# Kernel optimization log

Hardware: AMD Instinct MI355X
Metric: run time of the kernel (lower is better)

## Reference

```python
import jax, jax.numpy as jnp
import numpy as np

H = 16      # num_attention_heads
D = 1024    # hidden_size
HD = D // H # head dim = 64
ALPHA = 0.5


def setup_inputs() -> dict:
    key = jax.random.key(0)
    ks = jax.random.split(key, 12)
    B, S = 4, 1024
    s = 0.02
    return {
        "hidden_states": jax.random.normal(ks[0], (B, S, D), jnp.float32),
        "attention_mask": jnp.zeros((B, 1, 1, S), jnp.float32),
        "previous_attention": jax.random.uniform(ks[1], (B, H, S, S), jnp.float32),
        "Wq": jax.random.normal(ks[2], (D, D), jnp.float32) * s,
        "bq": jnp.zeros((D,), jnp.float32),
        "Wk": jax.random.normal(ks[3], (D, D), jnp.float32) * s,
        "bk": jnp.zeros((D,), jnp.float32),
        "Wv": jax.random.normal(ks[4], (D, D), jnp.float32) * s,
        "bv": jnp.zeros((D,), jnp.float32),
        "Wc": jax.random.normal(ks[5], (H, H), jnp.float32) * 0.25,  # 1x1 conv head-mix weight
        "bc": jnp.zeros((H,), jnp.float32),
    }


def reference(hidden_states, attention_mask, previous_attention,
              Wq, bq, Wk, bk, Wv, bv, Wc, bc):
    B, S, _ = hidden_states.shape

    def heads(x):  # [B,S,D] -> [B,H,S,HD]
        return x.reshape(B, S, H, HD).transpose(0, 2, 1, 3)

    q = heads(hidden_states @ Wq.T + bq)
    k = heads(hidden_states @ Wk.T + bk)
    v = heads(hidden_states @ Wv.T + bv)

    scores = jnp.einsum("bhsd,bhtd->bhst", q, k) / np.sqrt(HD).astype(np.float32)
    scores = scores + attention_mask
    probs = jax.nn.softmax(scores, axis=-1)

    # 1x1 conv across head channels == head-mixing matmul, then blend + re-softmax
    mixed_prev = jnp.einsum("gh,bhst->bgst", Wc, previous_attention) + bc[None, :, None, None]
    probs = jax.nn.softmax(ALPHA * mixed_prev + (1.0 - ALPHA) * probs, axis=-1)
    # dropout p=0.0 -> identity (inference)

    ctx = jnp.einsum("bhst,bhtd->bhsd", probs, v)
    ctx = ctx.transpose(0, 2, 1, 3).reshape(B, S, D)
    return ctx
```

## Files before the change

kernel.cpp:

```cpp
#include <hip/hip_runtime.h>
#include <hip/hip_bf16.h>

typedef unsigned short u16;
typedef __attribute__((ext_vector_type(8))) short  bf16x8;
typedef __attribute__((ext_vector_type(4))) float  f32x4;
typedef __attribute__((ext_vector_type(4))) int    i32x4;
typedef __attribute__((ext_vector_type(4))) float  f32x4v;

#define MFMA16(a,b,c) __builtin_amdgcn_mfma_f32_16x16x32_bf16((a),(b),(c),0,0,0)


static constexpr size_t OFF_HBF = 0;
static constexpr size_t OFF_WBF = 8388608;
static constexpr size_t OFF_QKV = 14680064;
static constexpr size_t OFF_VT  = 39845888;
static constexpr size_t OFF_MIX = 48234496;

__device__ __forceinline__ u16 f2b(float f) {
  unsigned int u = __builtin_bit_cast(unsigned int, f);
  unsigned int r = (u + 0x7fffu + ((u >> 16) & 1u)) >> 16;
  return (u16)r;
}
__device__ __forceinline__ float b2f(u16 x) {
  union { unsigned int u; float f; } c; c.u = ((unsigned int)x) << 16; return c.f;
}

__device__ __forceinline__ void gload_lds16(const u16* g, u16* l) {
  __builtin_amdgcn_global_load_lds(
      (const __attribute__((address_space(1))) unsigned int*)g,
      (__attribute__((address_space(3))) unsigned int*)l, 16, 0, 0);
}

__global__ void __launch_bounds__(256) k_convert(
    const float* __restrict__ hid, const float* __restrict__ wq,
    const float* __restrict__ wk,  const float* __restrict__ wv,
    u16* __restrict__ hbf, u16* __restrict__ wbf)
{
  int i4 = blockIdx.x * 256 + threadIdx.x;
  f32x4v v; u16* dst;
  if (i4 < 1048576) {
    v = *(const f32x4v*)(hid + (size_t)i4 * 4);
    dst = hbf + (size_t)i4 * 4;
  } else {
    int j = (i4 - 1048576) * 4;
    const float* s = (j < 1048576) ? (wq + j)
                   : (j < 2097152) ? (wk + (j - 1048576))
                                   : (wv + (j - 2097152));
    v = *(const f32x4v*)s;
    dst = wbf + j;
  }
  u16 o[4];
  for (int k = 0; k < 4; ++k) o[k] = f2b(v[k]);
  *(unsigned long long*)dst = *(unsigned long long*)o;
}

__global__ void __launch_bounds__(256) k_qkv(
    const u16* __restrict__ Abf, const u16* __restrict__ Wbf,
    const float* __restrict__ bq, const float* __restrict__ bk,
    const float* __restrict__ bv, u16* __restrict__ qkv)
{
  __shared__ __align__(16) u16 As[2][128][32];
  __shared__ __align__(16) u16 Bs[2][128][32];
  const int n0 = blockIdx.x * 128;
  const int m0 = blockIdx.y * 128;
  const int tid = threadIdx.x;
  const int l = tid & 63, w = tid >> 6;
  const int lr = l & 15, lg = l >> 4;
  const int wm = (w >> 1) * 64, wn = (w & 1) * 64;
  const int sx = (lg ^ ((lr >> 1) & 3)) * 8;

  f32x4 acc[4][4] = {};

  auto issue = [&](int buf, int k0) {
#pragma unroll
    for (int i = 0; i < 2; ++i) {
      int c = tid + i * 256;
      int row = c >> 2, cc = c & 3;
      int gc = cc ^ ((row >> 1) & 3);
      gload_lds16(Abf + (size_t)(m0 + row) * 1024 + k0 + gc * 8, &As[buf][row][cc * 8]);
      gload_lds16(Wbf + (size_t)(n0 + row) * 1024 + k0 + gc * 8, &Bs[buf][row][cc * 8]);
    }
  };

  issue(0, 0);
  for (int k0 = 0; k0 < 1024; k0 += 32) {
    int kb = (k0 >> 5) & 1;
    __syncthreads();
    if (k0 + 32 < 1024) issue(kb ^ 1, k0 + 32);
    bf16x8 a[4], bb[4];
#pragma unroll
    for (int mi = 0; mi < 4; ++mi)
      a[mi] = *(const bf16x8*)(&As[kb][wm + mi * 16 + lr][sx]);
#pragma unroll
    for (int ni = 0; ni < 4; ++ni)
      bb[ni] = *(const bf16x8*)(&Bs[kb][wn + ni * 16 + lr][sx]);
#pragma unroll
    for (int mi = 0; mi < 4; ++mi)
#pragma unroll
      for (int ni = 0; ni < 4; ++ni)
        acc[mi][ni] = MFMA16(a[mi], bb[ni], acc[mi][ni]);
  }
#pragma unroll
  for (int mi = 0; mi < 4; ++mi)
#pragma unroll
    for (int ni = 0; ni < 4; ++ni) {
      int col = n0 + wn + ni * 16 + lr;
      const float* bias = (col < 1024) ? bq : (col < 2048) ? bk : bv;
      float bvv = bias[col & 1023];
      int rowb = m0 + wm + mi * 16 + lg * 4;
#pragma unroll
      for (int r = 0; r < 4; ++r)
        qkv[(size_t)(rowb + r) * 3072 + col] = f2b(acc[mi][ni][r] + bvv);
    }
}

__global__ void __launch_bounds__(256) k_vt(const u16* __restrict__ qkv,
                                            u16* __restrict__ vt)
{
  __shared__ __align__(16) u16 tile[64][68];
  int blk = blockIdx.x;
  int st = blk & 15, h = (blk >> 4) & 15, b = blk >> 8;
  int tid = threadIdx.x;
  for (int i = 0; i < 16; ++i) {
    int idx = tid + i * 256;
    int r = idx >> 6, c = idx & 63;
    tile[r][c] = qkv[(size_t)(b * 1024 + st * 64 + r) * 3072 + 2048 + h * 64 + c];
  }
  __syncthreads();
  for (int i = 0; i < 16; ++i) {
    int idx = tid + i * 256;
    int d = idx >> 6, s = idx & 63;
    vt[((size_t)(b * 16 + h) * 64 + d) * 1024 + st * 64 + s] = tile[s][d];
  }
}

__global__ void __launch_bounds__(256) k_mix(
    const float* __restrict__ prev, const float* __restrict__ Wc,
    const float* __restrict__ bc, u16* __restrict__ mixed)
{
  __shared__ float wcs[256];
  __shared__ float bcs[16];
  int bsi = blockIdx.x;
  int b = bsi >> 10, s = bsi & 1023;
  int tid = threadIdx.x;
  wcs[tid] = 0.5f * Wc[tid];
  if (tid < 16) bcs[tid] = 0.5f * bc[tid];
  __syncthreads();
  size_t base = (size_t)b * 16777216 + (size_t)s * 1024;
  int t = tid * 4;
  f32x4v p[16];
#pragma unroll
  for (int hh = 0; hh < 16; ++hh)
    p[hh] = *(const f32x4v*)(prev + base + (size_t)hh * 1048576 + t);
#pragma unroll
  for (int g = 0; g < 16; ++g) {
    float bg = bcs[g];
    f32x4v a = {bg, bg, bg, bg};
#pragma unroll
    for (int hh = 0; hh < 16; ++hh)
      a += p[hh] * wcs[g * 16 + hh];
    u16 o[4];
#pragma unroll
    for (int j = 0; j < 4; ++j) o[j] = f2b(a[j]);
    *(unsigned long long*)(mixed + base + (size_t)g * 1048576 + t) =
        *(unsigned long long*)o;
  }
}

__global__ void __launch_bounds__(256) k_attn(
    const u16* __restrict__ qkv, const u16* __restrict__ vt,
    const u16* __restrict__ mixed, const float* __restrict__ mask,
    float* __restrict__ out)
{
  __shared__ __align__(16) char smraw[32768];
  u16   (*sc)[1024]   = (u16 (*)[1024])smraw;
  float (*ctxw)[16][64] = (float (*)[16][64])smraw;
  __shared__ float lw[4][16], l1inv[16];

  int blk = blockIdx.x;
  int sb = blk & 63, bh = blk >> 6;
  int h = bh & 15, b = bh >> 4;
  int s0 = sb * 16;
  int tid = threadIdx.x;
  int l = tid & 63, w = tid >> 6;
  int lr = l & 15, lg = l >> 4;

  const size_t qrow = (size_t)(b * 1024 + s0 + lr) * 3072 + h * 64;
  bf16x8 aq0 = *(const bf16x8*)(qkv + qrow + lg * 8);
  bf16x8 aq1 = *(const bf16x8*)(qkv + qrow + 32 + lg * 8);

#pragma unroll
  for (int tf = 0; tf < 16; ++tf) {
    int trow = w * 256 + tf * 16 + lr;
    const size_t krow = (size_t)(b * 1024 + trow) * 3072 + 1024 + h * 64;
    bf16x8 bk0 = *(const bf16x8*)(qkv + krow + lg * 8);
    bf16x8 bk1 = *(const bf16x8*)(qkv + krow + 32 + lg * 8);
    f32x4 acc = {0.f, 0.f, 0.f, 0.f};
    acc = MFMA16(aq0, bk0, acc);
    acc = MFMA16(aq1, bk1, acc);
    float mk = mask[b * 1024 + trow];
#pragma unroll
    for (int r = 0; r < 4; ++r) {
      int row = lg * 4 + r;
      float sv = acc[r] * 0.125f + mk;
      int addr = (((trow >> 3) ^ (row & 7)) << 3) + (trow & 7);
      sc[row][addr] = f2b(sv);
    }
  }
  __syncthreads();

  {
    int row = tid >> 4, ch = tid & 15;
    float sm = 0.f;
#pragma unroll
    for (int c8 = 0; c8 < 8; ++c8) {
      int chunk = ch * 8 + c8;
      bf16x8 v = *(const bf16x8*)(&sc[row][(chunk ^ (row & 7)) << 3]);
#pragma unroll
      for (int j = 0; j < 8; ++j) sm += __expf(b2f((u16)v[j]));
    }
    for (int d = 8; d >= 1; d >>= 1) sm += __shfl_xor(sm, d);
    if (ch == 0) l1inv[row] = 1.0f / sm;
  }
  __syncthreads();

  float l1h = 0.5f * l1inv[lr];
  float l2 = 0.f;
  f32x4 cacc[4] = {};
  const size_t mixrow = ((size_t)(b * 16 + h) * 1024 + s0 + lr) * 1024;
  const size_t vbase = (size_t)(b * 16 + h) * 64 * 1024;
  i32x4 mx_next = *(const i32x4*)(mixed + mixrow + w * 256 + lg * 8);
#pragma unroll
  for (int tt = 0; tt < 8; ++tt) {
    int tb = w * 256 + tt * 32 + lg * 8;
    i32x4 mx4 = mx_next;
    if (tt < 7) mx_next = *(const i32x4*)(mixed + mixrow + tb + 32);
    bf16x8 s8 = *(const bf16x8*)(&sc[lr][((tb >> 3) ^ (lr & 7)) << 3]);
    const u16* mxp = (const u16*)&mx4;
    bf16x8 pa;
    float ps = 0.f;
#pragma unroll
    for (int j = 0; j < 8; ++j) {
      float bl = b2f(mxp[j]) + __expf(b2f((u16)s8[j])) * l1h;
      float p = __expf(bl);
      ps += p;
      pa[j] = (short)f2b(p);
    }
    l2 += ps;
#pragma unroll
    for (int df = 0; df < 4; ++df) {
      bf16x8 vb = *(const bf16x8*)(vt + vbase + (size_t)(df * 16 + lr) * 1024 + tb);
      cacc[df] = MFMA16(pa, vb, cacc[df]);
    }
  }
  l2 += __shfl_xor(l2, 16);
  l2 += __shfl_xor(l2, 32);

  __syncthreads();
  if (lg == 0) lw[w][lr] = l2;
#pragma unroll
  for (int df = 0; df < 4; ++df)
#pragma unroll
    for (int r = 0; r < 4; ++r)
      ctxw[w][lg * 4 + r][df * 16 + lr] = cacc[df][r];
  __syncthreads();

  {
    int row = tid >> 4, d4 = (tid & 15) * 4;
    float den = lw[0][row] + lw[1][row] + lw[2][row] + lw[3][row];
    float inv = 1.0f / den;
    f32x4 o;
#pragma unroll
    for (int dd = 0; dd < 4; ++dd) {
      float a = ctxw[0][row][d4 + dd] + ctxw[1][row][d4 + dd] +
                ctxw[2][row][d4 + dd] + ctxw[3][row][d4 + dd];
      o[dd] = a * inv;
    }
    *(f32x4*)(out + ((size_t)(b * 1024 + s0 + row)) * 1024 + h * 64 + d4) = o;
  }
}

extern "C" void kernel_launch(void* const* d_in, const int* in_sizes, int n_in,
                              void* d_out, int out_size, void* d_ws, size_t ws_size,
                              hipStream_t stream) {
  const float* hidden = (const float*)d_in[0];
  const float* mask   = (const float*)d_in[1];
  const float* prev   = (const float*)d_in[2];
  const float* Wq     = (const float*)d_in[3];
  const float* bq     = (const float*)d_in[4];
  const float* Wk     = (const float*)d_in[5];
  const float* bk     = (const float*)d_in[6];
  const float* Wv     = (const float*)d_in[7];
  const float* bv     = (const float*)d_in[8];
  const float* Wc     = (const float*)d_in[9];
  const float* bc     = (const float*)d_in[10];
  float* out = (float*)d_out;
  char* ws = (char*)d_ws;

  u16* hbf   = (u16*)(ws + OFF_HBF);
  u16* wbf   = (u16*)(ws + OFF_WBF);
  u16* qkv   = (u16*)(ws + OFF_QKV);
  u16* vt    = (u16*)(ws + OFF_VT);
  u16* mixed = (u16*)(ws + OFF_MIX);

  k_convert<<<7168, 256, 0, stream>>>(hidden, Wq, Wk, Wv, hbf, wbf);
  k_qkv<<<dim3(24, 32), 256, 0, stream>>>(hbf, wbf, bq, bk, bv, qkv);
  k_vt<<<1024, 256, 0, stream>>>(qkv, vt);
  k_mix<<<4096, 256, 0, stream>>>(prev, Wc, bc, mixed);
  k_attn<<<4096, 256, 0, stream>>>(qkv, vt, mixed, mask, out);
}
```

Baseline: 598.5 us.

## Fuse V transpose into QKV GEMM epilogue, use exp2 softmax, prefetch mixed rows

The QKV GEMM epilogue now writes V straight into the transposed per-head layout, so the separate k_vt kernel and its extra pass over V are gone. The Q/K buffer stride shrinks from 3072 to 2048. Softmax switches to native exp2, with log2(e) folded into the score scale, the mask and the mix weights, which removes the multiply inside each exp. All eight mixed-attention loads in the attention loop are issued up front instead of one ahead. In exchange there are more live registers and scattered 8-byte V stores in the GEMM epilogue.

Measured after the change: 597.7 us. No clear change (-0.1%).

```diff
diff --git a/kernel.cpp b/kernel.cpp
--- a/kernel.cpp
+++ b/kernel.cpp
@@ -2,19 +2,25 @@
 #include <hip/hip_bf16.h>
 
 typedef unsigned short u16;
+typedef unsigned long long u64;
 typedef __attribute__((ext_vector_type(8))) short  bf16x8;
 typedef __attribute__((ext_vector_type(4))) float  f32x4;
 typedef __attribute__((ext_vector_type(4))) int    i32x4;
 typedef __attribute__((ext_vector_type(4))) float  f32x4v;
 
 #define MFMA16(a,b,c) __builtin_amdgcn_mfma_f32_16x16x32_bf16((a),(b),(c),0,0,0)
+#define EXP2(x) __builtin_amdgcn_exp2f(x)
 
 
 static constexpr size_t OFF_HBF = 0;
 static constexpr size_t OFF_WBF = 8388608;
 static constexpr size_t OFF_QKV = 14680064;
-static constexpr size_t OFF_VT  = 39845888;
-static constexpr size_t OFF_MIX = 48234496;
+static constexpr size_t OFF_VT  = 31457280;
+static constexpr size_t OFF_MIX = 39845888;
+
+static constexpr float LOG2E  = 1.44269504088896340736f;
+static constexpr float SSCALE = 0.125f * LOG2E;
+static constexpr float HALF2E = 0.5f * LOG2E;
 
 __device__ __forceinline__ u16 f2b(float f) {
   unsigned int u = __builtin_bit_cast(unsigned int, f);
@@ -51,13 +57,13 @@
   }
   u16 o[4];
   for (int k = 0; k < 4; ++k) o[k] = f2b(v[k]);
-  *(unsigned long long*)dst = *(unsigned long long*)o;
+  *(u64*)dst = *(u64*)o;
 }
 
 __global__ void __launch_bounds__(256) k_qkv(
     const u16* __restrict__ Abf, const u16* __restrict__ Wbf,
     const float* __restrict__ bq, const float* __restrict__ bk,
-    const float* __restrict__ bv, u16* __restrict__ qkv)
+    const float* __restrict__ bv, u16* __restrict__ qkv, u16* __restrict__ vt)
 {
   __shared__ __align__(16) u16 As[2][128][32];
   __shared__ __align__(16) u16 Bs[2][128][32];
@@ -108,30 +114,19 @@
       const float* bias = (col < 1024) ? bq : (col < 2048) ? bk : bv;
       float bvv = bias[col & 1023];
       int rowb = m0 + wm + mi * 16 + lg * 4;
-#pragma unroll
-      for (int r = 0; r < 4; ++r)
-        qkv[(size_t)(rowb + r) * 3072 + col] = f2b(acc[mi][ni][r] + bvv);
-    }
-}
-
-__global__ void __launch_bounds__(256) k_vt(const u16* __restrict__ qkv,
-                                            u16* __restrict__ vt)
-{
-  __shared__ __align__(16) u16 tile[64][68];
-  int blk = blockIdx.x;
-  int st = blk & 15, h = (blk >> 4) & 15, b = blk >> 8;
-  int tid = threadIdx.x;
-  for (int i = 0; i < 16; ++i) {
-    int idx = tid + i * 256;
-    int r = idx >> 6, c = idx & 63;
-    tile[r][c] = qkv[(size_t)(b * 1024 + st * 64 + r) * 3072 + 2048 + h * 64 + c];
-  }
-  __syncthreads();
-  for (int i = 0; i < 16; ++i) {
-    int idx = tid + i * 256;
-    int d = idx >> 6, s = idx & 63;
-    vt[((size_t)(b * 16 + h) * 64 + d) * 1024 + st * 64 + s] = tile[s][d];
-  }
+      if (col < 2048) {
+#pragma unroll
+        for (int r = 0; r < 4; ++r)
+          qkv[(size_t)(rowb + r) * 2048 + col] = f2b(acc[mi][ni][r] + bvv);
+      } else {
+        int hh = (col >> 6) & 15, d = col & 63;
+        int bb2 = rowb >> 10, sl = rowb & 1023;
+        u16 o[4];
+#pragma unroll
+        for (int r = 0; r < 4; ++r) o[r] = f2b(acc[mi][ni][r] + bvv);
+        *(u64*)(vt + ((size_t)(bb2 * 16 + hh) * 64 + d) * 1024 + sl) = *(u64*)o;
+      }
+    }
 }
 
 __global__ void __launch_bounds__(256) k_mix(
@@ -143,8 +138,8 @@
   int bsi = blockIdx.x;
   int b = bsi >> 10, s = bsi & 1023;
   int tid = threadIdx.x;
-  wcs[tid] = 0.5f * Wc[tid];
-  if (tid < 16) bcs[tid] = 0.5f * bc[tid];
+  wcs[tid] = HALF2E * Wc[tid];
+  if (tid < 16) bcs[tid] = HALF2E * bc[tid];
   __syncthreads();
   size_t base = (size_t)b * 16777216 + (size_t)s * 1024;
   int t = tid * 4;
@@ -162,8 +157,7 @@
     u16 o[4];
 #pragma unroll
     for (int j = 0; j < 4; ++j) o[j] = f2b(a[j]);
-    *(unsigned long long*)(mixed + base + (size_t)g * 1048576 + t) =
-        *(unsigned long long*)o;
+    *(u64*)(mixed + base + (size_t)g * 1048576 + t) = *(u64*)o;
   }
 }
 
@@ -185,24 +179,24 @@
   int l = tid & 63, w = tid >> 6;
   int lr = l & 15, lg = l >> 4;
 
-  const size_t qrow = (size_t)(b * 1024 + s0 + lr) * 3072 + h * 64;
+  const size_t qrow = (size_t)(b * 1024 + s0 + lr) * 2048 + h * 64;
   bf16x8 aq0 = *(const bf16x8*)(qkv + qrow + lg * 8);
   bf16x8 aq1 = *(const bf16x8*)(qkv + qrow + 32 + lg * 8);
 
 #pragma unroll
   for (int tf = 0; tf < 16; ++tf) {
     int trow = w * 256 + tf * 16 + lr;
-    const size_t krow = (size_t)(b * 1024 + trow) * 3072 + 1024 + h * 64;
+    const size_t krow = (size_t)(b * 1024 + trow) * 2048 + 1024 + h * 64;
     bf16x8 bk0 = *(const bf16x8*)(qkv + krow + lg * 8);
     bf16x8 bk1 = *(const bf16x8*)(qkv + krow + 32 + lg * 8);
     f32x4 acc = {0.f, 0.f, 0.f, 0.f};
     acc = MFMA16(aq0, bk0, acc);
     acc = MFMA16(aq1, bk1, acc);
-    float mk = mask[b * 1024 + trow];
+    float mk = mask[b * 1024 + trow] * LOG2E;
 #pragma unroll
     for (int r = 0; r < 4; ++r) {
       int row = lg * 4 + r;
-      float sv = acc[r] * 0.125f + mk;
+      float sv = acc[r] * SSCALE + mk;
       int addr = (((trow >> 3) ^ (row & 7)) << 3) + (trow & 7);
       sc[row][addr] = f2b(sv);
     }
@@ -217,32 +211,33 @@
       int chunk = ch * 8 + c8;
       bf16x8 v = *(const bf16x8*)(&sc[row][(chunk ^ (row & 7)) << 3]);
 #pragma unroll
-      for (int j = 0; j < 8; ++j) sm += __expf(b2f((u16)v[j]));
+      for (int j = 0; j < 8; ++j) sm += EXP2(b2f((u16)v[j]));
     }
     for (int d = 8; d >= 1; d >>= 1) sm += __shfl_xor(sm, d);
     if (ch == 0) l1inv[row] = 1.0f / sm;
   }
   __syncthreads();
 
-  float l1h = 0.5f * l1inv[lr];
+  float l1h = HALF2E * l1inv[lr];
   float l2 = 0.f;
   f32x4 cacc[4] = {};
   const size_t mixrow = ((size_t)(b * 16 + h) * 1024 + s0 + lr) * 1024;
   const size_t vbase = (size_t)(b * 16 + h) * 64 * 1024;
-  i32x4 mx_next = *(const i32x4*)(mixed + mixrow + w * 256 + lg * 8);
+  i32x4 mxa[8];
+#pragma unroll
+  for (int tt = 0; tt < 8; ++tt)
+    mxa[tt] = *(const i32x4*)(mixed + mixrow + w * 256 + tt * 32 + lg * 8);
 #pragma unroll
   for (int tt = 0; tt < 8; ++tt) {
     int tb = w * 256 + tt * 32 + lg * 8;
-    i32x4 mx4 = mx_next;
-    if (tt < 7) mx_next = *(const i32x4*)(mixed + mixrow + tb + 32);
     bf16x8 s8 = *(const bf16x8*)(&sc[lr][((tb >> 3) ^ (lr & 7)) << 3]);
-    const u16* mxp = (const u16*)&mx4;
+    const u16* mxp = (const u16*)&mxa[tt];
     bf16x8 pa;
     float ps = 0.f;
 #pragma unroll
     for (int j = 0; j < 8; ++j) {
-      float bl = b2f(mxp[j]) + __expf(b2f((u16)s8[j])) * l1h;
-      float p = __expf(bl);
+      float bl = b2f(mxp[j]) + EXP2(b2f((u16)s8[j])) * l1h;
+      float p = EXP2(bl);
       ps += p;
       pa[j] = (short)f2b(p);
     }
@@ -304,8 +299,7 @@
   u16* mixed = (u16*)(ws + OFF_MIX);
 
   k_convert<<<7168, 256, 0, stream>>>(hidden, Wq, Wk, Wv, hbf, wbf);
-  k_qkv<<<dim3(24, 32), 256, 0, stream>>>(hbf, wbf, bq, bk, bv, qkv);
-  k_vt<<<1024, 256, 0, stream>>>(qkv, vt);
+  k_qkv<<<dim3(24, 32), 256, 0, stream>>>(hbf, wbf, bq, bk, bv, qkv, vt);
   k_mix<<<4096, 256, 0, stream>>>(prev, Wc, bc, mixed);
   k_attn<<<4096, 256, 0, stream>>>(qkv, vt, mixed, mask, out);
 }
```
